# Kernel tuning notes

Measured on AMD Instinct MI355X. Metric: run time of the kernel, lower is better.

## Reference

```python
import jax, jax.numpy as jnp
import numpy as np

N_NODES = 100000
N_EDGES = 1600000
NODE_DIM = 128
EDGE_DIM = 64
HID = 64
N_POSTS = 10000


def _gru_cell(x, h, w_ih, w_hh, b_ih, b_hh):
    # torch.nn.GRUCell semantics
    gi = x @ w_ih.T + b_ih          # [N, 3H]
    gh = h @ w_hh.T + b_hh          # [N, 3H]
    i_r, i_z, i_n = jnp.split(gi, 3, axis=-1)
    h_r, h_z, h_n = jnp.split(gh, 3, axis=-1)
    r = jax.nn.sigmoid(i_r + h_r)
    z = jax.nn.sigmoid(i_z + h_z)
    n = jnp.tanh(i_n + r * h_n)
    return (1.0 - z) * n + z * h


def setup_inputs() -> dict:
    key = jax.random.key(0)
    ks = jax.random.split(key, 20)
    s = 0.05
    f32 = jnp.float32
    return {
        "node_features": jax.random.normal(ks[0], (N_NODES, NODE_DIM), dtype=f32),
        "edge_attr": jax.random.normal(ks[1], (N_EDGES, EDGE_DIM), dtype=f32),
        "edge_index": jax.random.randint(ks[2], (2, N_EDGES), 0, N_NODES),
        "post_mask": jax.random.randint(ks[3], (N_POSTS,), 0, N_NODES),
        "n_layers": 2,
        # node_encoder
        "W_node": jax.random.normal(ks[4], (HID, NODE_DIM), dtype=f32) * s,
        "b_node": jnp.zeros((HID,), dtype=f32),
        # edge_encoder
        "W_edge": jax.random.normal(ks[5], (HID, EDGE_DIM), dtype=f32) * s,
        "b_edge": jnp.zeros((HID,), dtype=f32),
        # message_aggregator: Linear(2H -> H)
        "W_agg": jax.random.normal(ks[6], (HID, 2 * HID), dtype=f32) * s,
        "b_agg": jnp.zeros((HID,), dtype=f32),
        # GRUCell(H, H)
        "w_ih": jax.random.normal(ks[7], (3 * HID, HID), dtype=f32) * s,
        "w_hh": jax.random.normal(ks[8], (3 * HID, HID), dtype=f32) * s,
        "b_ih": jnp.zeros((3 * HID,), dtype=f32),
        "b_hh": jnp.zeros((3 * HID,), dtype=f32),
        # output MLP: H -> H//2 -> 1
        "W_out1": jax.random.normal(ks[9], (HID // 2, HID), dtype=f32) * s,
        "b_out1": jnp.zeros((HID // 2,), dtype=f32),
        "W_out2": jax.random.normal(ks[10], (1, HID // 2), dtype=f32) * s,
        "b_out2": jnp.zeros((1,), dtype=f32),
    }


def reference(node_features, edge_attr, edge_index, post_mask, n_layers,
              W_node, b_node, W_edge, b_edge, W_agg, b_agg,
              w_ih, w_hh, b_ih, b_hh, W_out1, b_out1, W_out2, b_out2):
    h = jax.nn.relu(node_features @ W_node.T + b_node)       # [N, H]
    e = jax.nn.relu(edge_attr @ W_edge.T + b_edge)           # [E, H]
    src, dst = edge_index[0], edge_index[1]
    for _ in range(int(n_layers)):
        # batched gather-concat-linear (replaces per-edge python loop)
        msg = jnp.concatenate([h[src], e], axis=1) @ W_agg.T + b_agg  # [E, H]
        messages = jax.ops.segment_sum(msg, dst, num_segments=N_NODES)  # scatter-add
        h = _gru_cell(messages, h, w_ih, w_hh, b_ih, b_hh)
    p = h[post_mask]                                          # [P, H]
    logits = (jax.nn.relu(p @ W_out1.T + b_out1) @ W_out2.T + b_out2).squeeze(-1)
    return jax.nn.sigmoid(logits)
```

## Files before the change

### kernel.cpp

```cpp
#include <hip/hip_runtime.h>

using short8  = __attribute__((ext_vector_type(8))) short;
using ushort8 = __attribute__((ext_vector_type(8))) unsigned short;
using f32x4   = __attribute__((ext_vector_type(4))) float;

static __device__ __forceinline__ short f2bf(float f) {
  unsigned u = __float_as_uint(f);
  u += 0x7fffu + ((u >> 16) & 1u);
  return (short)(u >> 16);
}
static __device__ __forceinline__ float bf2f(short s) {
  return __uint_as_float(((unsigned)(unsigned short)s) << 16);
}
static __device__ __forceinline__ float us2f(unsigned short s) {
  return __uint_as_float(((unsigned)s) << 16);
}
static __device__ __forceinline__ short8 load8_bf16(const float* __restrict__ p) {
  const f32x4* q = (const f32x4*)p;
  f32x4 a = q[0], b = q[1];
  short8 r;
  r[0]=f2bf(a[0]); r[1]=f2bf(a[1]); r[2]=f2bf(a[2]); r[3]=f2bf(a[3]);
  r[4]=f2bf(b[0]); r[5]=f2bf(b[1]); r[6]=f2bf(b[2]); r[7]=f2bf(b[3]);
  return r;
}
static __device__ __forceinline__ void split8(const float* p, short8& hi, short8& lo) {
  const f32x4* q = (const f32x4*)p;
  f32x4 a = q[0], b = q[1];
  float v[8] = {a[0],a[1],a[2],a[3],b[0],b[1],b[2],b[3]};
#pragma unroll
  for (int j = 0; j < 8; ++j) {
    short h = f2bf(v[j]);
    hi[j] = h;
    lo[j] = f2bf(v[j] - bf2f(h));
  }
}

__global__ __launch_bounds__(256) void node_encode(
    const float* __restrict__ X, const float* __restrict__ Wn,
    const float* __restrict__ bn, float* __restrict__ h,
    unsigned short* __restrict__ hb, int nNodes) {
  int tid = threadIdx.x, lane = tid & 63, w = tid >> 6, lg = lane >> 4, lr = lane & 15;
  short8 bf[4][4];
#pragma unroll
  for (int t = 0; t < 4; ++t)
#pragma unroll
    for (int kk = 0; kk < 4; ++kk)
      bf[t][kk] = load8_bf16(Wn + (t*16+lr)*128 + kk*32 + lg*8);
  float bias[4];
#pragma unroll
  for (int t = 0; t < 4; ++t) bias[t] = bn[t*16+lr];

  int base = blockIdx.x * 64 + w * 16;
  int arow = base + lr;
  int nn = arow < nNodes ? arow : nNodes - 1;
  f32x4 acc[4] = {};
#pragma unroll
  for (int kk = 0; kk < 4; ++kk) {
    short8 aH, aL;
    split8(X + (size_t)nn*128 + kk*32 + lg*8, aH, aL);
#pragma unroll
    for (int t = 0; t < 4; ++t) {
      acc[t] = __builtin_amdgcn_mfma_f32_16x16x32_bf16(aH, bf[t][kk], acc[t], 0, 0, 0);
      acc[t] = __builtin_amdgcn_mfma_f32_16x16x32_bf16(aL, bf[t][kk], acc[t], 0, 0, 0);
    }
  }
#pragma unroll
  for (int t = 0; t < 4; ++t)
#pragma unroll
    for (int i = 0; i < 4; ++i) {
      int orow = base + lg*4 + i;
      if (orow < nNodes) {
        float v = fmaxf(acc[t][i] + bias[t], 0.f);
        h[(size_t)orow*64 + t*16 + lr] = v;
        hb[(size_t)orow*64 + t*16 + lr] = (unsigned short)f2bf(v);
      }
    }
}

__global__ __launch_bounds__(256) void hist_deg(
    const int* __restrict__ dst, int* __restrict__ deg, int nEdges) {
  for (int e = blockIdx.x*256 + threadIdx.x; e < nEdges; e += gridDim.x*256)
    atomicAdd(&deg[dst[e]], 1);
}

__global__ __launch_bounds__(256) void scan_pass1(
    const int* __restrict__ deg, int* __restrict__ bsum, int n) {
  int b = blockIdx.x, tid = threadIdx.x;
  int base = b * 4096;
  int s = 0;
  for (int j = tid; j < 4096; j += 256) {
    int i = base + j;
    s += (i < n) ? deg[i] : 0;
  }
  __shared__ int ws[4];
#pragma unroll
  for (int o = 32; o; o >>= 1) s += __shfl_down(s, o);
  if ((tid & 63) == 0) ws[tid >> 6] = s;
  __syncthreads();
  if (tid == 0) bsum[b] = ws[0] + ws[1] + ws[2] + ws[3];
}

__global__ void scan_pass2(const int* __restrict__ bsum, int* __restrict__ boff,
                           int* __restrict__ off, int nBlocks, int n) {
  if (threadIdx.x == 0 && blockIdx.x == 0) {
    int run = 0;
    for (int b = 0; b < nBlocks; ++b) { boff[b] = run; run += bsum[b]; }
    off[n] = run;
  }
}

__global__ __launch_bounds__(256) void scan_pass3(
    const int* __restrict__ deg, const int* __restrict__ boff,
    int* __restrict__ off, int n) {
  int b = blockIdx.x, tid = threadIdx.x;
  int lane = tid & 63, w = tid >> 6;
  int base = b * 4096 + tid * 16;
  int d[16], tot = 0;
#pragma unroll
  for (int j = 0; j < 16; ++j) {
    d[j] = (base + j < n) ? deg[base + j] : 0;
    tot += d[j];
  }
  int s = tot;
#pragma unroll
  for (int o = 1; o < 64; o <<= 1) {
    int t = __shfl_up(s, o);
    if (lane >= o) s += t;
  }
  __shared__ int ws[4];
  if (lane == 63) ws[w] = s;
  __syncthreads();
  int wo = 0;
  for (int k = 0; k < 4; ++k) wo += (k < w) ? ws[k] : 0;
  int run = boff[b] + wo + s - tot;
#pragma unroll
  for (int j = 0; j < 16; ++j) {
    if (base + j < n) off[base + j] = run;
    run += d[j];
  }
}

__global__ __launch_bounds__(256) void fill_csr(
    const int* __restrict__ src, const int* __restrict__ dst,
    const int* __restrict__ off, int* __restrict__ cursor,
    int* __restrict__ srcs, int* __restrict__ pos2, int nEdges) {
  for (int e = blockIdx.x*256 + threadIdx.x; e < nEdges; e += gridDim.x*256) {
    int d = dst[e];
    int pos = off[d] + atomicAdd(&cursor[d], 1);
    srcs[pos] = src[e];
    pos2[e] = pos;
  }
}

__global__ __launch_bounds__(256) void edge_mlp(
    const float* __restrict__ EA, const float* __restrict__ We,
    const float* __restrict__ be, const int* __restrict__ pos2,
    unsigned short* __restrict__ encb, int nEdges) {
  __shared__ float tile[128][66];
  int tid = threadIdx.x, lane = tid & 63, w = tid >> 6;
  int lr = lane & 15, lg = lane >> 4;

  short8 bf[4][2];
#pragma unroll
  for (int t = 0; t < 4; ++t)
#pragma unroll
    for (int kk = 0; kk < 2; ++kk)
      bf[t][kk] = load8_bf16(We + (t*16+lr)*64 + kk*32 + lg*8);
  float bias[4];
#pragma unroll
  for (int t = 0; t < 4; ++t) bias[t] = be[t*16+lr];

  int e0 = blockIdx.x * 128;
  int r0 = e0 + w*32 + lr;
  int c0 = r0 < nEdges ? r0 : nEdges - 1;
  int c1 = (r0+16) < nEdges ? (r0+16) : nEdges - 1;
  const float* p0 = EA + (size_t)c0*64;
  const float* p1 = EA + (size_t)c1*64;
  short8 aH[2][2], aL[2][2];
#pragma unroll
  for (int kk = 0; kk < 2; ++kk) {
    split8(p0 + kk*32 + lg*8, aH[0][kk], aL[0][kk]);
    split8(p1 + kk*32 + lg*8, aH[1][kk], aL[1][kk]);
  }
  f32x4 acc[2][4] = {};
#pragma unroll
  for (int b = 0; b < 2; ++b)
#pragma unroll
    for (int kk = 0; kk < 2; ++kk)
#pragma unroll
      for (int t = 0; t < 4; ++t) {
        acc[b][t] = __builtin_amdgcn_mfma_f32_16x16x32_bf16(aH[b][kk], bf[t][kk], acc[b][t], 0,0,0);
        acc[b][t] = __builtin_amdgcn_mfma_f32_16x16x32_bf16(aL[b][kk], bf[t][kk], acc[b][t], 0,0,0);
      }
#pragma unroll
  for (int b = 0; b < 2; ++b)
#pragma unroll
    for (int t = 0; t < 4; ++t)
#pragma unroll
      for (int i = 0; i < 4; ++i)
        tile[w*32 + b*16 + lg*4 + i][t*16 + lr] = fmaxf(acc[b][t][i] + bias[t], 0.f);
  int er = lane >> 3, fs = lane & 7;
#pragma unroll
  for (int it = 0; it < 4; ++it) {
    int r = w*32 + it*8 + er;
    int e = e0 + r;
    if (e < nEdges) {
      int p = pos2[e];
      const float* tp = &tile[r][fs*8];
      ushort8 v;
#pragma unroll
      for (int q = 0; q < 8; ++q) v[q] = (unsigned short)f2bf(tp[q]);
      *(ushort8*)(encb + (size_t)p*64 + fs*8) = v;
    }
  }
}

__global__ __launch_bounds__(256) void seg_sum(
    const unsigned short* __restrict__ encb, const int* __restrict__ off,
    float* __restrict__ Esum, int nNodes) {
  int tid = threadIdx.x, lane = tid & 63, w = tid >> 6;
  int er = lane >> 3, fs = lane & 7;
  int n0 = (blockIdx.x * 4 + w) * 4;
  if (n0 >= nNodes) return;
  int a[4], b[4];
#pragma unroll
  for (int j = 0; j < 4; ++j) {
    int n = n0 + j;
    a[j] = (n < nNodes) ? off[n] : 0;
    b[j] = (n < nNodes) ? off[n + 1] : 0;
  }
  float acc[4][8];
#pragma unroll
  for (int j = 0; j < 4; ++j)
#pragma unroll
    for (int q = 0; q < 8; ++q) acc[j][q] = 0.f;
  int mx = 0;
#pragma unroll
  for (int j = 0; j < 4; ++j) { int c = b[j] - a[j]; if (c > mx) mx = c; }
  for (int t = 0; t < mx; t += 8) {
#pragma unroll
    for (int j = 0; j < 4; ++j) {
      int i0 = a[j] + t + er;
      if (i0 < b[j]) {
        ushort8 v = *(const ushort8*)(encb + (size_t)i0*64 + fs*8);
#pragma unroll
        for (int q = 0; q < 8; ++q) acc[j][q] += us2f(v[q]);
      }
    }
  }
#pragma unroll
  for (int j = 0; j < 4; ++j)
#pragma unroll
    for (int q = 0; q < 8; ++q) {
      float v = acc[j][q];
      v += __shfl_xor(v, 8);
      v += __shfl_xor(v, 16);
      v += __shfl_xor(v, 32);
      acc[j][q] = v;
    }
  if (er == 0) {
#pragma unroll
    for (int j = 0; j < 4; ++j) {
      int n = n0 + j;
      if (n < nNodes) {
        f32x4 lo = {acc[j][0], acc[j][1], acc[j][2], acc[j][3]};
        f32x4 hi = {acc[j][4], acc[j][5], acc[j][6], acc[j][7]};
        *(f32x4*)(Esum + (size_t)n * 64 + fs * 8) = lo;
        *(f32x4*)(Esum + (size_t)n * 64 + fs * 8 + 4) = hi;
      }
    }
  }
}

__global__ __launch_bounds__(256) void make_combos(
    const float* __restrict__ wih, const float* __restrict__ Wagg,
    const float* __restrict__ bagg, const float* __restrict__ whh,
    short* __restrict__ WceH, short* __restrict__ WceL,
    short* __restrict__ WchH, short* __restrict__ WchL,
    short* __restrict__ whhH, short* __restrict__ whhL, float* __restrict__ bihA) {
  int idx = blockIdx.x*256 + threadIdx.x;
  if (idx < 12288) {
    int r = idx >> 6, k = idx & 63;
    float a = 0.f, b = 0.f;
    for (int j = 0; j < 64; ++j) {
      float ww = wih[r*64 + j];
      a += ww * Wagg[j*128 + k];
      b += ww * Wagg[j*128 + 64 + k];
    }
    short ah = f2bf(a);
    WchH[idx] = ah; WchL[idx] = f2bf(a - bf2f(ah));
    short bh = f2bf(b);
    WceH[idx] = bh; WceL[idx] = f2bf(b - bf2f(bh));
    float wv = whh[idx];
    short hh = f2bf(wv);
    whhH[idx] = hh; whhL[idx] = f2bf(wv - bf2f(hh));
    if (idx < 192) {
      float s = 0.f;
      for (int j = 0; j < 64; ++j) s += wih[idx*64 + j] * bagg[j];
      bihA[idx] = s;
    }
  }
}

__global__ __launch_bounds__(256) void gather_G(
    const unsigned short* __restrict__ hb, const int* __restrict__ off,
    const int* __restrict__ srcs, float* __restrict__ G, int nNodes) {
  int tid = threadIdx.x, lane = tid & 63, w = tid >> 6;
  int er = lane >> 3, fs = lane & 7;
  int n0 = (blockIdx.x * 4 + w) * 4;
  if (n0 >= nNodes) return;
  int a[4], b[4];
#pragma unroll
  for (int j = 0; j < 4; ++j) {
    int n = n0 + j;
    a[j] = (n < nNodes) ? off[n] : 0;
    b[j] = (n < nNodes) ? off[n + 1] : 0;
  }
  float acc[4][8];
#pragma unroll
  for (int j = 0; j < 4; ++j)
#pragma unroll
    for (int q = 0; q < 8; ++q) acc[j][q] = 0.f;
  int mx = 0;
#pragma unroll
  for (int j = 0; j < 4; ++j) { int c = b[j] - a[j]; if (c > mx) mx = c; }
  for (int t = 0; t < mx; t += 16) {
    int s0[4], s1[4];
    bool m0[4], m1[4];
#pragma unroll
    for (int j = 0; j < 4; ++j) {
      int i0 = a[j] + t + er, i1 = i0 + 8;
      int bm = b[j] - 1;
      m0[j] = i0 < b[j]; m1[j] = i1 < b[j];
      int c0 = m0[j] ? i0 : (bm > a[j] ? bm : a[j]);
      int c1 = m1[j] ? i1 : c0;
      s0[j] = (b[j] > a[j]) ? srcs[c0] : 0;
      s1[j] = (b[j] > a[j]) ? srcs[c1] : 0;
    }
#pragma unroll
    for (int j = 0; j < 4; ++j) {
      ushort8 v0 = *(const ushort8*)(hb + (size_t)s0[j] * 64 + fs * 8);
      ushort8 v1 = *(const ushort8*)(hb + (size_t)s1[j] * 64 + fs * 8);
      if (m0[j]) {
#pragma unroll
        for (int q = 0; q < 8; ++q) acc[j][q] += us2f(v0[q]);
      }
      if (m1[j]) {
#pragma unroll
        for (int q = 0; q < 8; ++q) acc[j][q] += us2f(v1[q]);
      }
    }
  }
#pragma unroll
  for (int j = 0; j < 4; ++j)
#pragma unroll
    for (int q = 0; q < 8; ++q) {
      float v = acc[j][q];
      v += __shfl_xor(v, 8);
      v += __shfl_xor(v, 16);
      v += __shfl_xor(v, 32);
      acc[j][q] = v;
    }
  if (er == 0) {
#pragma unroll
    for (int j = 0; j < 4; ++j) {
      int n = n0 + j;
      if (n < nNodes) {
        f32x4 lo = {acc[j][0], acc[j][1], acc[j][2], acc[j][3]};
        f32x4 hi = {acc[j][4], acc[j][5], acc[j][6], acc[j][7]};
        *(f32x4*)(G + (size_t)n * 64 + fs * 8) = lo;
        *(f32x4*)(G + (size_t)n * 64 + fs * 8 + 4) = hi;
      }
    }
  }
}

__global__ __launch_bounds__(256) void layer_dense(
    const float* __restrict__ h_old, const float* __restrict__ Esum,
    const float* __restrict__ G, const int* __restrict__ deg,
    const short* __restrict__ WceH, const short* __restrict__ WceL,
    const short* __restrict__ WchH, const short* __restrict__ WchL,
    const short* __restrict__ whhH, const short* __restrict__ whhL,
    const float* __restrict__ bihA, const float* __restrict__ bih,
    const float* __restrict__ bhh, float* __restrict__ h_new,
    unsigned short* __restrict__ h_newb, int nNodes) {
  int tid = threadIdx.x, lane = tid & 63, w = tid >> 6;
  int lr = lane & 15, lg = lane >> 4;
  int nb = blockIdx.x * 64;

  int arow = nb + w*16 + lr; if (arow >= nNodes) arow = nNodes - 1;
  short8 EsH[2], EsL[2], GHf[2], GLf[2], HH[2], HL[2];
#pragma unroll
  for (int kk = 0; kk < 2; ++kk) {
    split8(Esum + (size_t)arow*64 + kk*32 + lg*8, EsH[kk], EsL[kk]);
    split8(G + (size_t)arow*64 + kk*32 + lg*8, GHf[kk], GLf[kk]);
    split8(h_old + (size_t)arow*64 + kk*32 + lg*8, HH[kk], HL[kk]);
  }

  int row0 = nb + w*16 + lg*4;
  float degv[4];
#pragma unroll
  for (int i = 0; i < 4; ++i) {
    int n = row0 + i;
    degv[i] = (n < nNodes) ? (float)deg[n] : 0.f;
  }

  f32x4 gi[12], gh[12];
#pragma unroll
  for (int ct = 0; ct < 12; ++ct) {
    float bi = bih[ct*16 + lr], ba = bihA[ct*16 + lr], bh = bhh[ct*16 + lr];
#pragma unroll
    for (int i = 0; i < 4; ++i) { gi[ct][i] = bi + degv[i]*ba; gh[ct][i] = bh; }
  }

#pragma unroll
  for (int ct = 0; ct < 12; ++ct) {
    int wb = (ct*16 + lr)*64 + lg*8;
#pragma unroll
    for (int kk = 0; kk < 2; ++kk) {
      int o = wb + kk*32;
      short8 wceh = *(const short8*)(WceH + o);
      short8 wcel = *(const short8*)(WceL + o);
      short8 wchh = *(const short8*)(WchH + o);
      short8 wchl = *(const short8*)(WchL + o);
      short8 whh_h = *(const short8*)(whhH + o);
      short8 whh_l = *(const short8*)(whhL + o);
      gi[ct] = __builtin_amdgcn_mfma_f32_16x16x32_bf16(EsH[kk], wceh, gi[ct], 0,0,0);
      gi[ct] = __builtin_amdgcn_mfma_f32_16x16x32_bf16(EsL[kk], wceh, gi[ct], 0,0,0);
      gi[ct] = __builtin_amdgcn_mfma_f32_16x16x32_bf16(EsH[kk], wcel, gi[ct], 0,0,0);
      gi[ct] = __builtin_amdgcn_mfma_f32_16x16x32_bf16(GHf[kk], wchh, gi[ct], 0,0,0);
      gi[ct] = __builtin_amdgcn_mfma_f32_16x16x32_bf16(GLf[kk], wchh, gi[ct], 0,0,0);
      gi[ct] = __builtin_amdgcn_mfma_f32_16x16x32_bf16(GHf[kk], wchl, gi[ct], 0,0,0);
      gh[ct] = __builtin_amdgcn_mfma_f32_16x16x32_bf16(HH[kk], whh_h, gh[ct], 0,0,0);
      gh[ct] = __builtin_amdgcn_mfma_f32_16x16x32_bf16(HL[kk], whh_h, gh[ct], 0,0,0);
      gh[ct] = __builtin_amdgcn_mfma_f32_16x16x32_bf16(HH[kk], whh_l, gh[ct], 0,0,0);
    }
  }

#pragma unroll
  for (int ct = 0; ct < 4; ++ct)
#pragma unroll
    for (int i = 0; i < 4; ++i) {
      int n = row0 + i;
      if (n < nNodes) {
        int jh = ct*16 + lr;
        float r = 1.f/(1.f + expf(-(gi[ct][i] + gh[ct][i])));
        float z = 1.f/(1.f + expf(-(gi[ct+4][i] + gh[ct+4][i])));
        float nn = tanhf(gi[ct+8][i] + r * gh[ct+8][i]);
        float hv = h_old[(size_t)n*64 + jh];
        float hn = (1.f - z)*nn + z*hv;
        h_new[(size_t)n*64 + jh] = hn;
        h_newb[(size_t)n*64 + jh] = (unsigned short)f2bf(hn);
      }
    }
}

__global__ __launch_bounds__(256) void out_mlp(
    const float* __restrict__ h, const int* __restrict__ pm,
    const float* __restrict__ W1, const float* __restrict__ b1,
    const float* __restrict__ W2, const float* __restrict__ b2,
    float* __restrict__ out, int nPosts) {
  int tid = threadIdx.x;
  int lane = tid & 63;
  int p = blockIdx.x*4 + (tid >> 6);
  if (p >= nPosts) return;
  int n = pm[p];
  float v = h[(size_t)n*64 + lane];
  int row = lane & 31;
  float o = b1[row];
#pragma unroll
  for (int k = 0; k < 64; ++k) {
    float vb = __shfl(v, k);
    o += vb * W1[row*64 + k];
  }
  o = fmaxf(o, 0.f);
  float val = o * W2[row] * 0.5f;
#pragma unroll
  for (int offm = 32; offm > 0; offm >>= 1) val += __shfl_xor(val, offm);
  if (lane == 0) out[p] = 1.f/(1.f + expf(-(val + b2[0])));
}

static inline char* aln(char*& w, size_t bytes) {
  uintptr_t p = ((uintptr_t)w + 255) & ~(uintptr_t)255;
  char* r = (char*)p;
  w = r + bytes;
  return r;
}

extern "C" void kernel_launch(void* const* d_in, const int* in_sizes, int n_in,
                              void* d_out, int out_size, void* d_ws, size_t ws_size,
                              hipStream_t stream) {
  const float* X    = (const float*)d_in[0];
  const float* EA   = (const float*)d_in[1];
  const int*   EI   = (const int*)d_in[2];
  const int*   PM   = (const int*)d_in[3];
  const float* Wn   = (const float*)d_in[5];
  const float* bn   = (const float*)d_in[6];
  const float* We   = (const float*)d_in[7];
  const float* be   = (const float*)d_in[8];
  const float* Wagg = (const float*)d_in[9];
  const float* bagg = (const float*)d_in[10];
  const float* wih  = (const float*)d_in[11];
  const float* whh  = (const float*)d_in[12];
  const float* bih  = (const float*)d_in[13];
  const float* bhh  = (const float*)d_in[14];
  const float* W1   = (const float*)d_in[15];
  const float* b1   = (const float*)d_in[16];
  const float* W2   = (const float*)d_in[17];
  const float* b2   = (const float*)d_in[18];
  float* out = (float*)d_out;

  int nNodes = in_sizes[0] / 128;
  int nEdges = in_sizes[1] / 64;
  int nPosts = in_sizes[3];
  const int* src = EI;
  const int* dst = EI + nEdges;
  int nSB = (nNodes + 4095) / 4096;

  char* w = (char*)d_ws;
  float* h0   = (float*)aln(w, (size_t)nNodes * 64 * 4);
  float* h1   = (float*)aln(w, (size_t)nNodes * 64 * 4);
  unsigned short* h0b = (unsigned short*)aln(w, (size_t)nNodes * 64 * 2);
  unsigned short* h1b = (unsigned short*)aln(w, (size_t)nNodes * 64 * 2);
  float* Esum = (float*)aln(w, (size_t)nNodes * 64 * 4);
  float* G    = (float*)aln(w, (size_t)nNodes * 64 * 4);
  short* WceH = (short*)aln(w, 12288 * 2);
  short* WceL = (short*)aln(w, 12288 * 2);
  short* WchH = (short*)aln(w, 12288 * 2);
  short* WchL = (short*)aln(w, 12288 * 2);
  short* whhH = (short*)aln(w, 12288 * 2);
  short* whhL = (short*)aln(w, 12288 * 2);
  float* bihA = (float*)aln(w, 192 * 4);
  int*   off  = (int*)aln(w, (size_t)(nNodes + 1) * 4);
  int*   deg  = (int*)aln(w, (size_t)nNodes * 4);
  int*   cur  = (int*)aln(w, (size_t)nNodes * 4);
  int*   srcs = (int*)aln(w, (size_t)nEdges * 4);
  int*   pos2 = (int*)aln(w, (size_t)nEdges * 4);
  int*   bsum = (int*)aln(w, (size_t)nSB * 4);
  int*   boff = (int*)aln(w, (size_t)nSB * 4);
  unsigned short* encb = (unsigned short*)aln(w, (size_t)nEdges * 64 * 2);

  hipMemsetAsync(deg, 0, (size_t)nNodes * 4, stream);
  hipMemsetAsync(cur, 0, (size_t)nNodes * 4, stream);

  hist_deg<<<2048, 256, 0, stream>>>(dst, deg, nEdges);
  scan_pass1<<<nSB, 256, 0, stream>>>(deg, bsum, nNodes);
  scan_pass2<<<1, 1, 0, stream>>>(bsum, boff, off, nSB, nNodes);
  scan_pass3<<<nSB, 256, 0, stream>>>(deg, boff, off, nNodes);
  fill_csr<<<2048, 256, 0, stream>>>(src, dst, off, cur, srcs, pos2, nEdges);

  node_encode<<<(nNodes + 63) / 64, 256, 0, stream>>>(X, Wn, bn, h0, h0b, nNodes);
  edge_mlp<<<(nEdges + 127) / 128, 256, 0, stream>>>(EA, We, be, pos2, encb, nEdges);
  seg_sum<<<(nNodes + 15) / 16, 256, 0, stream>>>(encb, off, Esum, nNodes);
  make_combos<<<48, 256, 0, stream>>>(wih, Wagg, bagg, whh,
                                      WceH, WceL, WchH, WchL, whhH, whhL, bihA);

  gather_G<<<(nNodes + 15) / 16, 256, 0, stream>>>(h0b, off, srcs, G, nNodes);
  layer_dense<<<(nNodes + 63) / 64, 256, 0, stream>>>(
      h0, Esum, G, deg, WceH, WceL, WchH, WchL, whhH, whhL,
      bihA, bih, bhh, h1, h1b, nNodes);
  gather_G<<<(nNodes + 15) / 16, 256, 0, stream>>>(h1b, off, srcs, G, nNodes);
  layer_dense<<<(nNodes + 63) / 64, 256, 0, stream>>>(
      h1, Esum, G, deg, WceH, WceL, WchH, WchL, whhH, whhL,
      bihA, bih, bhh, h0, h0b, nNodes);

  out_mlp<<<(nPosts + 3) / 4, 256, 0, stream>>>(h0, PM, W1, b1, W2, b2, out, nPosts);
}
```

Measured before the change: 865.8 us.

## Fuse CSR fill into edge MLP and drop hi/lo split with permuted layout

Removes the separate fill_csr kernel and the pos2 array. Each edge_mlp wave now does the atomic cursor increment and srcs write itself, then shuffles each edge's CSR position to the lanes that write its output row. Each lane stores its MFMA outputs straight to encb as 4 permuted bf16 values, with no LDS tile. The hi/lo split of edge attributes is replaced by a single bf16 MFMA pass, halving the MFMA work at some cost in precision. To compensate for the permuted encb column order, WceH/WceL columns are permuted in make_combos, which relies on seg_sum passing the order through unchanged.

Measured after the change: 827.3 us. 4.5% less time.

```diff
diff --git a/kernel.cpp b/kernel.cpp
--- a/kernel.cpp
+++ b/kernel.cpp
@@ -2,6 +2,7 @@
 
 using short8  = __attribute__((ext_vector_type(8))) short;
 using ushort8 = __attribute__((ext_vector_type(8))) unsigned short;
+using us4     = __attribute__((ext_vector_type(4))) unsigned short;
 using f32x4   = __attribute__((ext_vector_type(4))) float;
 
 static __device__ __forceinline__ short f2bf(float f) {
@@ -140,23 +141,12 @@
   }
 }
 
-__global__ __launch_bounds__(256) void fill_csr(
-    const int* __restrict__ src, const int* __restrict__ dst,
-    const int* __restrict__ off, int* __restrict__ cursor,
-    int* __restrict__ srcs, int* __restrict__ pos2, int nEdges) {
-  for (int e = blockIdx.x*256 + threadIdx.x; e < nEdges; e += gridDim.x*256) {
-    int d = dst[e];
-    int pos = off[d] + atomicAdd(&cursor[d], 1);
-    srcs[pos] = src[e];
-    pos2[e] = pos;
-  }
-}
-
 __global__ __launch_bounds__(256) void edge_mlp(
     const float* __restrict__ EA, const float* __restrict__ We,
-    const float* __restrict__ be, const int* __restrict__ pos2,
+    const float* __restrict__ be, const int* __restrict__ src,
+    const int* __restrict__ dst, const int* __restrict__ off,
+    int* __restrict__ cur, int* __restrict__ srcs,
     unsigned short* __restrict__ encb, int nEdges) {
-  __shared__ float tile[128][66];
   int tid = threadIdx.x, lane = tid & 63, w = tid >> 6;
   int lr = lane & 15, lg = lane >> 4;
 
@@ -170,49 +160,47 @@
 #pragma unroll
   for (int t = 0; t < 4; ++t) bias[t] = be[t*16+lr];
 
-  int e0 = blockIdx.x * 128;
-  int r0 = e0 + w*32 + lr;
-  int c0 = r0 < nEdges ? r0 : nEdges - 1;
-  int c1 = (r0+16) < nEdges ? (r0+16) : nEdges - 1;
-  const float* p0 = EA + (size_t)c0*64;
-  const float* p1 = EA + (size_t)c1*64;
-  short8 aH[2][2], aL[2][2];
+  int e0 = blockIdx.x * 128 + w * 32;
+  int pos_reg = 0;
+  if (lane < 32) {
+    int e = e0 + lane;
+    if (e < nEdges) {
+      int d = dst[e];
+      pos_reg = off[d] + atomicAdd(&cur[d], 1);
+      srcs[pos_reg] = src[e];
+    }
+  }
+
+  int c0 = e0 + lr;      if (c0 >= nEdges) c0 = nEdges - 1;
+  int c1 = e0 + 16 + lr; if (c1 >= nEdges) c1 = nEdges - 1;
+  const float* p0 = EA + (size_t)c0 * 64;
+  const float* p1 = EA + (size_t)c1 * 64;
+  f32x4 acc[2][4] = {};
 #pragma unroll
   for (int kk = 0; kk < 2; ++kk) {
-    split8(p0 + kk*32 + lg*8, aH[0][kk], aL[0][kk]);
-    split8(p1 + kk*32 + lg*8, aH[1][kk], aL[1][kk]);
-  }
-  f32x4 acc[2][4] = {};
+    short8 a0 = load8_bf16(p0 + kk*32 + lg*8);
+    short8 a1 = load8_bf16(p1 + kk*32 + lg*8);
+#pragma unroll
+    for (int t = 0; t < 4; ++t) {
+      acc[0][t] = __builtin_amdgcn_mfma_f32_16x16x32_bf16(a0, bf[t][kk], acc[0][t], 0,0,0);
+      acc[1][t] = __builtin_amdgcn_mfma_f32_16x16x32_bf16(a1, bf[t][kk], acc[1][t], 0,0,0);
+    }
+  }
 #pragma unroll
   for (int b = 0; b < 2; ++b)
 #pragma unroll
-    for (int kk = 0; kk < 2; ++kk)
-#pragma unroll
-      for (int t = 0; t < 4; ++t) {
-        acc[b][t] = __builtin_amdgcn_mfma_f32_16x16x32_bf16(aH[b][kk], bf[t][kk], acc[b][t], 0,0,0);
-        acc[b][t] = __builtin_amdgcn_mfma_f32_16x16x32_bf16(aL[b][kk], bf[t][kk], acc[b][t], 0,0,0);
-      }
-#pragma unroll
-  for (int b = 0; b < 2; ++b)
-#pragma unroll
-    for (int t = 0; t < 4; ++t)
-#pragma unroll
-      for (int i = 0; i < 4; ++i)
-        tile[w*32 + b*16 + lg*4 + i][t*16 + lr] = fmaxf(acc[b][t][i] + bias[t], 0.f);
-  int er = lane >> 3, fs = lane & 7;
-#pragma unroll
-  for (int it = 0; it < 4; ++it) {
-    int r = w*32 + it*8 + er;
-    int e = e0 + r;
-    if (e < nEdges) {
-      int p = pos2[e];
-      const float* tp = &tile[r][fs*8];
-      ushort8 v;
-#pragma unroll
-      for (int q = 0; q < 8; ++q) v[q] = (unsigned short)f2bf(tp[q]);
-      *(ushort8*)(encb + (size_t)p*64 + fs*8) = v;
-    }
-  }
+    for (int i = 0; i < 4; ++i) {
+      int rloc = b*16 + lg*4 + i;
+      int e = e0 + rloc;
+      int pos = __shfl(pos_reg, rloc);
+      if (e < nEdges) {
+        us4 v;
+#pragma unroll
+        for (int t = 0; t < 4; ++t)
+          v[t] = (unsigned short)f2bf(fmaxf(acc[b][t][i] + bias[t], 0.f));
+        *(us4*)(encb + (size_t)pos*64 + lr*4) = v;
+      }
+    }
 }
 
 __global__ __launch_bounds__(256) void seg_sum(
@@ -289,8 +277,9 @@
     }
     short ah = f2bf(a);
     WchH[idx] = ah; WchL[idx] = f2bf(a - bf2f(ah));
+    int kp = (k & 15) * 4 + (k >> 4);
     short bh = f2bf(b);
-    WceH[idx] = bh; WceL[idx] = f2bf(b - bf2f(bh));
+    WceH[r*64 + kp] = bh; WceL[r*64 + kp] = f2bf(b - bf2f(bh));
     float wv = whh[idx];
     short hh = f2bf(wv);
     whhH[idx] = hh; whhL[idx] = f2bf(wv - bf2f(hh));
@@ -535,7 +524,6 @@
   int*   deg  = (int*)aln(w, (size_t)nNodes * 4);
   int*   cur  = (int*)aln(w, (size_t)nNodes * 4);
   int*   srcs = (int*)aln(w, (size_t)nEdges * 4);
-  int*   pos2 = (int*)aln(w, (size_t)nEdges * 4);
   int*   bsum = (int*)aln(w, (size_t)nSB * 4);
   int*   boff = (int*)aln(w, (size_t)nSB * 4);
   unsigned short* encb = (unsigned short*)aln(w, (size_t)nEdges * 64 * 2);
@@ -547,10 +535,10 @@
   scan_pass1<<<nSB, 256, 0, stream>>>(deg, bsum, nNodes);
   scan_pass2<<<1, 1, 0, stream>>>(bsum, boff, off, nSB, nNodes);
   scan_pass3<<<nSB, 256, 0, stream>>>(deg, boff, off, nNodes);
-  fill_csr<<<2048, 256, 0, stream>>>(src, dst, off, cur, srcs, pos2, nEdges);
 
   node_encode<<<(nNodes + 63) / 64, 256, 0, stream>>>(X, Wn, bn, h0, h0b, nNodes);
-  edge_mlp<<<(nEdges + 127) / 128, 256, 0, stream>>>(EA, We, be, pos2, encb, nEdges);
+  edge_mlp<<<(nEdges + 127) / 128, 256, 0, stream>>>(EA, We, be, src, dst, off, cur,
+                                                     srcs, encb, nEdges);
   seg_sum<<<(nNodes + 15) / 16, 256, 0, stream>>>(encb, off, Esum, nNodes);
   make_combos<<<48, 256, 0, stream>>>(wih, Wagg, bagg, whh,
                                       WceH, WceL, WchH, WchL, whhH, whhL, bihA);
```
